# Kernel tuning notes

Measured on AMD Instinct MI355X. Metric: run time of the kernel, lower is better.

## Reference

```python
import jax, jax.numpy as jnp
import numpy as np

NEG_SLOPE = 0.2


def _segment_softmax(logits, seg, num_segments):
    m = jax.ops.segment_max(logits, seg, num_segments=num_segments)
    m = jnp.where(jnp.isfinite(m), m, 0.0)
    e = jnp.exp(logits - m[seg])
    s = jax.ops.segment_sum(e, seg, num_segments=num_segments)
    return e / (s[seg] + 1e-16)


def _gat_conv(x, src, dst, W, a_src, a_dst, b, num_nodes):
    # PyG GATConv, heads=1, concat=True, add_self_loops already applied to src/dst.
    h = x @ W                                  # [N, F_out]
    alpha_src = h @ a_src                      # [N]
    alpha_dst = h @ a_dst                      # [N]
    logits = jax.nn.leaky_relu(alpha_src[src] + alpha_dst[dst], NEG_SLOPE)  # [E]
    alpha = _segment_softmax(logits, dst, num_nodes)                        # [E]
    out = jax.ops.segment_sum(alpha[:, None] * h[src], dst, num_segments=num_nodes)
    return out + b


def setup_inputs() -> dict:
    key = jax.random.key(0)
    ks = jax.random.split(key, 16)
    N, E, F_in = 50000, 1600000, 256
    x = jax.random.normal(ks[0], (N, F_in), dtype=jnp.float32)
    edge_index = jax.random.randint(ks[1], (2, E), 0, N, dtype=jnp.int64)
    edge_attr = jax.random.normal(ks[2], (E, 1), dtype=jnp.float32)

    def glorot(k, shape):
        fan = sum(shape) if len(shape) > 1 else shape[0]
        return jax.random.normal(k, shape, dtype=jnp.float32) * jnp.sqrt(2.0 / fan)

    params = {
        "W1": glorot(ks[3], (F_in, 48)), "as1": glorot(ks[4], (48,)),
        "ad1": glorot(ks[5], (48,)),     "b1": jnp.zeros((48,), jnp.float32),
        "W2": glorot(ks[6], (48, 60)),   "as2": glorot(ks[7], (60,)),
        "ad2": glorot(ks[8], (60,)),     "b2": jnp.zeros((60,), jnp.float32),
        "W3": glorot(ks[9], (60, 1)),    "as3": glorot(ks[10], (1,)),
        "ad3": glorot(ks[11], (1,)),     "b3": jnp.zeros((1,), jnp.float32),
    }
    return {"x": x, "edge_index": edge_index, "edge_attr": edge_attr, **params}


def reference(x, edge_index, edge_attr, W1, as1, ad1, b1, W2, as2, ad2, b2, W3, as3, ad3, b3):
    # edge_attr is accepted but ignored: GATConv was built without edge_dim, so no lin_edge.
    N = x.shape[0]
    loops = jnp.arange(N, dtype=edge_index.dtype)
    src = jnp.concatenate([edge_index[0], loops])  # add_self_loops=True
    dst = jnp.concatenate([edge_index[1], loops])
    h = jax.nn.relu(_gat_conv(x, src, dst, W1, as1, ad1, b1, N))
    h = jax.nn.relu(_gat_conv(h, src, dst, W2, as2, ad2, b2, N))
    h = _gat_conv(h, src, dst, W3, as3, ad3, b3, N)
    return h.reshape(-1)  # flatten -> [N]
```

## Files before the change

kernel.cpp:

```cpp
#include <hip/hip_runtime.h>
#include <cstdint>
#include <cstddef>


__device__ __forceinline__ float leaky(float v) { return v > 0.f ? v : 0.2f * v; }

__device__ __forceinline__ unsigned short f2bf(float x) {
    unsigned int u = __float_as_uint(x);
    u = (u + 0x7FFFu + ((u >> 16) & 1u)) >> 16;
    return (unsigned short)u;
}
__device__ __forceinline__ float bf2f(unsigned short b) {
    return __uint_as_float(((unsigned int)b) << 16);
}

typedef _Float16 half8 __attribute__((ext_vector_type(8)));
typedef float f32x4 __attribute__((ext_vector_type(4)));

#define BSHIFT 7
#define BCAP   5120
#define CTILE  8192


__global__ __launch_bounds__(256) void coarse_bin_kernel(
    const int* __restrict__ ei, unsigned int* __restrict__ staged,
    int* __restrict__ gcursor, int E, int K) {
    __shared__ int hist[512];
    __shared__ int rank[512];
    __shared__ int base[512];
    for (int b = threadIdx.x; b < K; b += 256) { hist[b] = 0; rank[b] = 0; }
    __syncthreads();

    int e0 = blockIdx.x * CTILE;
    int e1 = min(E, e0 + CTILE);

    for (int e = e0 + threadIdx.x; e < e1; e += 256) {
        int d = ei[E + e];
        atomicAdd(&hist[d >> BSHIFT], 1);
    }
    __syncthreads();

    for (int b = threadIdx.x; b < K; b += 256) {
        int c = hist[b];
        base[b] = c ? atomicAdd(&gcursor[b], c) : 0;
    }
    __syncthreads();

    for (int e = e0 + threadIdx.x; e < e1; e += 256) {
        int s = ei[e];
        int d = ei[E + e];
        int b = d >> BSHIFT;
        int r = atomicAdd(&rank[b], 1);
        staged[(size_t)b * BCAP + base[b] + r] =
            ((unsigned int)(d & ((1 << BSHIFT) - 1)) << 16) | (unsigned int)s;
    }
}


__global__ __launch_bounds__(512) void bucket_scan_kernel(
    const int* __restrict__ gcursor, int* __restrict__ bbase, int K) {
    __shared__ int sh[512];
    int t = threadIdx.x;
    int v = (t < K) ? gcursor[t] : 0;
    sh[t] = v;
    __syncthreads();
    for (int off = 1; off < 512; off <<= 1) {
        int a = (t >= off) ? sh[t - off] : 0;
        __syncthreads();
        sh[t] += a;
        __syncthreads();
    }
    if (t < K) bbase[t] = sh[t] - v;
}


__global__ __launch_bounds__(256) void fine_sort_kernel(
    const unsigned int* __restrict__ staged, const int* __restrict__ gcursor,
    const int* __restrict__ bbase, int* __restrict__ rowptr, int* __restrict__ csr,
    int N, int E) {
    __shared__ int cnt[128];
    __shared__ int off[128];
    __shared__ int lcsr[BCAP];
    const int b = blockIdx.x;
    const int t = threadIdx.x;
    const int c = gcursor[b];
    const int gb = bbase[b];
    const unsigned int* rec = staged + (size_t)b * BCAP;

    if (t < 128) cnt[t] = 0;
    __syncthreads();

    for (int i = t; i < c; i += 256) atomicAdd(&cnt[rec[i] >> 16], 1);
    __syncthreads();

    if (t < 128) off[t] = cnt[t];
    __syncthreads();
    for (int s = 1; s < 128; s <<= 1) {
        int a = (t >= s && t < 128) ? off[t - s] : 0;
        __syncthreads();
        if (t < 128) off[t] += a;
        __syncthreads();
    }

    if (t < 128) {
        int excl = off[t] - cnt[t];
        int n = (b << BSHIFT) + t;
        if (n <= N) rowptr[n] = gb + excl;
        cnt[t] = excl;
    }
    if (b == 0 && t == 0) rowptr[N] = E;
    __syncthreads();

    for (int i = t; i < c; i += 256) {
        unsigned int r = rec[i];
        int p = atomicAdd(&cnt[r >> 16], 1);
        lcsr[p] = (int)(r & 0xFFFFu);
    }
    __syncthreads();

    for (int i = t; i < c; i += 256) csr[gb + i] = lcsr[i];
}


template <int FIN>
__global__ __launch_bounds__(256) void gemm1_mfma_kernel(
    const float* __restrict__ X, const float* __restrict__ W,
    const float* __restrict__ avs, const float* __restrict__ avd,
    unsigned short* __restrict__ hb, float* __restrict__ asrc, float* __restrict__ adst,
    int N) {
    constexpr int FOUT = 48;
    constexpr int KK = FIN / 32;
    static_assert(FIN % 32 == 0, "FIN multiple of 32");

    const int wid  = __builtin_amdgcn_readfirstlane(threadIdx.x >> 6);
    const int lane = threadIdx.x & 63;
    const int col  = lane & 15;
    const int grp  = lane >> 4;
    const int wbase = blockIdx.x * 64 + wid * 16;

    int arow = wbase + col;
    if (arow >= N) arow = N - 1;
    const float* xrow = X + (size_t)arow * FIN + grp * 8;

    half8 Bf[3][KK];
#pragma unroll
    for (int t = 0; t < 3; t++) {
#pragma unroll
        for (int kk = 0; kk < KK; kk++) {
            const float* wp = W + (size_t)(kk * 32 + grp * 8) * FOUT + t * 16 + col;
#pragma unroll
            for (int j = 0; j < 8; j++)
                Bf[t][kk][j] = (_Float16)wp[(size_t)j * FOUT];
        }
    }

    f32x4 acc0 = {0.f, 0.f, 0.f, 0.f};
    f32x4 acc1 = {0.f, 0.f, 0.f, 0.f};
    f32x4 acc2 = {0.f, 0.f, 0.f, 0.f};

#pragma unroll
    for (int kk = 0; kk < KK; kk++) {
        float4 xa = *(const float4*)(xrow + kk * 32);
        float4 xb = *(const float4*)(xrow + kk * 32 + 4);
        float xs[8] = {xa.x, xa.y, xa.z, xa.w, xb.x, xb.y, xb.z, xb.w};
        half8 ah, al;
#pragma unroll
        for (int j = 0; j < 8; j++) {
            _Float16 h = (_Float16)xs[j];
            ah[j] = h;
            al[j] = (_Float16)(xs[j] - (float)h);
        }
        acc0 = __builtin_amdgcn_mfma_f32_16x16x32_f16(ah, Bf[0][kk], acc0, 0, 0, 0);
        acc1 = __builtin_amdgcn_mfma_f32_16x16x32_f16(ah, Bf[1][kk], acc1, 0, 0, 0);
        acc2 = __builtin_amdgcn_mfma_f32_16x16x32_f16(ah, Bf[2][kk], acc2, 0, 0, 0);
        acc0 = __builtin_amdgcn_mfma_f32_16x16x32_f16(al, Bf[0][kk], acc0, 0, 0, 0);
        acc1 = __builtin_amdgcn_mfma_f32_16x16x32_f16(al, Bf[1][kk], acc1, 0, 0, 0);
        acc2 = __builtin_amdgcn_mfma_f32_16x16x32_f16(al, Bf[2][kk], acc2, 0, 0, 0);
    }

    float avs0 = avs[col], avs1 = avs[16 + col], avs2 = avs[32 + col];
    float avd0 = avd[col], avd1 = avd[16 + col], avd2 = avd[32 + col];

#pragma unroll
    for (int r = 0; r < 4; r++) {
        float ps = acc0[r] * avs0 + acc1[r] * avs1 + acc2[r] * avs2;
        float pd = acc0[r] * avd0 + acc1[r] * avd1 + acc2[r] * avd2;
#pragma unroll
        for (int off = 8; off; off >>= 1) {
            ps += __shfl_xor(ps, off, 64);
            pd += __shfl_xor(pd, off, 64);
        }
        int nd = wbase + grp * 4 + r;
        if (col == r && nd < N) { asrc[nd] = ps; adst[nd] = pd; }
    }

#pragma unroll
    for (int r = 0; r < 4; r++) {
        int nd = wbase + grp * 4 + r;
        if (nd < N) {
            unsigned short* hp = hb + (size_t)nd * 64 + col;
            hp[0]  = f2bf(acc0[r]);
            hp[16] = f2bf(acc1[r]);
            hp[32] = f2bf(acc2[r]);
        }
    }
}


template <int FIN, int FOUT, int FT>
__global__ __launch_bounds__(256) void gemm_sgpr_kernel(
    const float* __restrict__ X, const float* __restrict__ W,
    const float* __restrict__ avs, const float* __restrict__ avd,
    unsigned short* __restrict__ hb, float* __restrict__ asrc, float* __restrict__ adst,
    int N) {
    static_assert(4 * FT == FOUT, "FT must be FOUT/4");
    __shared__ float red[2][4][64];

    const int wid  = __builtin_amdgcn_readfirstlane(threadIdx.x >> 6);
    const int lane = threadIdx.x & 63;
    const int n    = blockIdx.x * 64 + lane;
    const int nc   = (n < N) ? n : N - 1;
    const int fbase = wid * FT;

    const float* xrow = X + (size_t)nc * FIN;

    float acc[FT];
#pragma unroll
    for (int c = 0; c < FT; c++) acc[c] = 0.f;

#pragma unroll
    for (int k = 0; k < FIN; k += 4) {
        float4 xv = *(const float4*)(xrow + k);
        const float* w0 = W + (size_t)k * FOUT + fbase;
#pragma unroll
        for (int c = 0; c < FT; c++) {
            acc[c] = fmaf(xv.x, w0[c],            acc[c]);
            acc[c] = fmaf(xv.y, w0[FOUT + c],     acc[c]);
            acc[c] = fmaf(xv.z, w0[2 * FOUT + c], acc[c]);
            acc[c] = fmaf(xv.w, w0[3 * FOUT + c], acc[c]);
        }
    }

    float ps = 0.f, pd = 0.f;
#pragma unroll
    for (int c = 0; c < FT; c++) {
        ps = fmaf(acc[c], avs[fbase + c], ps);
        pd = fmaf(acc[c], avd[fbase + c], pd);
    }
    red[0][wid][lane] = ps;
    red[1][wid][lane] = pd;

    if (n < N) {
        if constexpr ((FT & 1) == 0) {
            unsigned int* dst = (unsigned int*)(hb + (size_t)n * 64 + fbase);
#pragma unroll
            for (int c = 0; c < FT; c += 2) {
                unsigned int pk = (unsigned int)f2bf(acc[c]) |
                                  ((unsigned int)f2bf(acc[c + 1]) << 16);
                dst[c >> 1] = pk;
            }
        } else {
#pragma unroll
            for (int c = 0; c < FT; c++)
                hb[(size_t)n * 64 + fbase + c] = f2bf(acc[c]);
        }
    }

    __syncthreads();
    if (threadIdx.x < 64 && n < N) {
        float s = red[0][0][lane] + red[0][1][lane] + red[0][2][lane] + red[0][3][lane];
        float d = red[1][0][lane] + red[1][1][lane] + red[1][2][lane] + red[1][3][lane];
        asrc[n] = s;
        adst[n] = d;
    }
}


#define CHUNK 128

template <int FOUT, bool RELU>
__global__ __launch_bounds__(256) void agg_bf16_kernel(
    const int* __restrict__ rowptr, const int* __restrict__ csr,
    const float* __restrict__ asrc, const float* __restrict__ adst,
    const unsigned short* __restrict__ hb, const float* __restrict__ bias,
    float* __restrict__ OUT, int N) {
    __shared__ int2 wslds[4][CHUNK];
    const int wv = threadIdx.x >> 6;
    int n = blockIdx.x * 4 + wv;
    if (n >= N) return;
    const int lane = threadIdx.x & 63;
    const int rs = rowptr[n], re = rowptr[n + 1];
    const float ad_n = adst[n];
    const float wself = __expf(leaky(asrc[n] + ad_n));
    const int fc = (lane < FOUT) ? lane : FOUT - 1;

    float acc = wself * bf2f(hb[(size_t)n * 64 + fc]);
    float wpart = 0.f;

    for (int base = rs; base < re; base += CHUNK) {
        const int cnt = min(CHUNK, re - base);
        if (lane < cnt) {
            int s = csr[base + lane];
            float w = __expf(leaky(asrc[s] + ad_n));
            wpart += w;
            wslds[wv][lane] = make_int2(s, __float_as_int(w));
        }
        int i = 0;
        for (; i + 8 <= cnt; i += 8) {
            int2 p[8];
#pragma unroll
            for (int u = 0; u < 8; u++) p[u] = wslds[wv][i + u];
            float hv[8];
#pragma unroll
            for (int u = 0; u < 8; u++) hv[u] = bf2f(hb[(size_t)p[u].x * 64 + fc]);
#pragma unroll
            for (int u = 0; u < 8; u++) acc = fmaf(__int_as_float(p[u].y), hv[u], acc);
        }
        for (; i < cnt; i++) {
            int2 pp = wslds[wv][i];
            acc = fmaf(__int_as_float(pp.y), bf2f(hb[(size_t)pp.x * 64 + fc]), acc);
        }
    }

#pragma unroll
    for (int off = 32; off; off >>= 1) wpart += __shfl_xor(wpart, off, 64);
    float ssum = wpart + wself;

    if (lane < FOUT) {
        float o = acc / (ssum + 1e-16f) + bias[lane];
        if (RELU) o = fmaxf(o, 0.f);
        OUT[(size_t)n * FOUT + lane] = o;
    }
}


__global__ __launch_bounds__(256) void agg_bf16_h3_kernel(
    const int* __restrict__ rowptr, const int* __restrict__ csr,
    const float* __restrict__ asrc, const float* __restrict__ adst,
    const unsigned short* __restrict__ hb, const float* __restrict__ bias,
    const float* __restrict__ W3, float* __restrict__ h3, int N) {
    constexpr int FOUT = 60;
    __shared__ int2 wslds[4][CHUNK];
    const int wv = threadIdx.x >> 6;
    int n = blockIdx.x * 4 + wv;
    if (n >= N) return;
    const int lane = threadIdx.x & 63;
    const int rs = rowptr[n], re = rowptr[n + 1];
    const float ad_n = adst[n];
    const float wself = __expf(leaky(asrc[n] + ad_n));
    const int fc = (lane < FOUT) ? lane : FOUT - 1;

    float acc = wself * bf2f(hb[(size_t)n * 64 + fc]);
    float wpart = 0.f;

    for (int base = rs; base < re; base += CHUNK) {
        const int cnt = min(CHUNK, re - base);
        if (lane < cnt) {
            int s = csr[base + lane];
            float w = __expf(leaky(asrc[s] + ad_n));
            wpart += w;
            wslds[wv][lane] = make_int2(s, __float_as_int(w));
        }
        int i = 0;
        for (; i + 8 <= cnt; i += 8) {
            int2 p[8];
#pragma unroll
            for (int u = 0; u < 8; u++) p[u] = wslds[wv][i + u];
            float hv[8];
#pragma unroll
            for (int u = 0; u < 8; u++) hv[u] = bf2f(hb[(size_t)p[u].x * 64 + fc]);
#pragma unroll
            for (int u = 0; u < 8; u++) acc = fmaf(__int_as_float(p[u].y), hv[u], acc);
        }
        for (; i < cnt; i++) {
            int2 pp = wslds[wv][i];
            acc = fmaf(__int_as_float(pp.y), bf2f(hb[(size_t)pp.x * 64 + fc]), acc);
        }
    }

#pragma unroll
    for (int off = 32; off; off >>= 1) wpart += __shfl_xor(wpart, off, 64);
    float ssum = wpart + wself;

    float t = 0.f;
    if (lane < FOUT) {
        float o = fmaxf(acc / (ssum + 1e-16f) + bias[lane], 0.f);
        t = o * W3[lane];
    }
#pragma unroll
    for (int off = 32; off; off >>= 1) t += __shfl_xor(t, off, 64);
    if (lane == 0) h3[n] = t;
}


__global__ __launch_bounds__(256) void agg1_kernel(
    const int* __restrict__ rowptr, const int* __restrict__ csr,
    const float* __restrict__ h3,
    const float* __restrict__ as3p, const float* __restrict__ ad3p,
    const float* __restrict__ bias, float* __restrict__ OUT, int N) {
    int n = blockIdx.x * 4 + (threadIdx.x >> 6);
    if (n >= N) return;
    int lane = threadIdx.x & 63;
    int rs = rowptr[n], re = rowptr[n + 1];
    const float a_s = as3p[0];
    float hn = h3[n];
    float adn = ad3p[0] * hn;
    float wself = __expf(leaky(a_s * hn + adn));

    float ssum = 0.f, accv = 0.f;
    for (int e = rs + lane; e < re; e += 64) {
        float hs = h3[csr[e]];
        float w = __expf(leaky(a_s * hs + adn));
        ssum += w;
        accv = fmaf(w, hs, accv);
    }
#pragma unroll
    for (int off = 32; off; off >>= 1) {
        ssum += __shfl_xor(ssum, off, 64);
        accv += __shfl_xor(accv, off, 64);
    }
    ssum += wself;
    accv = fmaf(wself, hn, accv);
    if (lane == 0) OUT[n] = accv / (ssum + 1e-16f) + bias[0];
}


extern "C" void kernel_launch(void* const* d_in, const int* in_sizes, int n_in,
                              void* d_out, int out_size, void* d_ws, size_t ws_size,
                              hipStream_t stream) {
    const float* x      = (const float*)d_in[0];
    const int*   ei     = (const int*)d_in[1];
    const float* W1  = (const float*)d_in[3];
    const float* as1 = (const float*)d_in[4];
    const float* ad1 = (const float*)d_in[5];
    const float* b1  = (const float*)d_in[6];
    const float* W2  = (const float*)d_in[7];
    const float* as2 = (const float*)d_in[8];
    const float* ad2 = (const float*)d_in[9];
    const float* b2  = (const float*)d_in[10];
    const float* W3  = (const float*)d_in[11];
    const float* as3 = (const float*)d_in[12];
    const float* ad3 = (const float*)d_in[13];
    const float* b3  = (const float*)d_in[14];

    const int N = in_sizes[0] / 256;
    const int E = in_sizes[1] / 2;
    const int K = (N + (1 << BSHIFT) - 1) >> BSHIFT;

    char* p = (char*)d_ws;
    auto alloc = [&](size_t bytes) -> void* {
        void* r = (void*)p;
        p += ((bytes + 255) / 256) * 256;
        return r;
    };
    int*   gcursor = (int*)alloc(512 * 4);
    int*   bbase   = (int*)alloc(512 * 4);
    int*   rowptr  = (int*)alloc(((size_t)N + 1) * 4);
    int*   csr     = (int*)alloc((size_t)E * 4);
    unsigned short* hb = (unsigned short*)alloc((size_t)N * 64 * 2);
    float* actbuf  = (float*)alloc((size_t)N * 48 * 4);
    float* h3      = (float*)alloc((size_t)N * 4);
    float* asrc    = (float*)alloc((size_t)N * 4);
    float* adst    = (float*)alloc((size_t)N * 4);
    unsigned int* staged = (unsigned int*)actbuf;

    hipMemsetAsync(gcursor, 0, 512 * 4, stream);
    int cblocks = (E + CTILE - 1) / CTILE;
    coarse_bin_kernel<<<cblocks, 256, 0, stream>>>(ei, staged, gcursor, E, K);
    bucket_scan_kernel<<<1, 512, 0, stream>>>(gcursor, bbase, K);
    fine_sort_kernel<<<K, 256, 0, stream>>>(staged, gcursor, bbase, rowptr, csr, N, E);

    int gblocks = (N + 63) / 64;
    int ablocks = (N + 3) / 4;

    gemm1_mfma_kernel<256><<<gblocks, 256, 0, stream>>>(
        x, W1, as1, ad1, hb, asrc, adst, N);
    agg_bf16_kernel<48, true><<<ablocks, 256, 0, stream>>>(rowptr, csr, asrc, adst, hb, b1, actbuf, N);

    gemm_sgpr_kernel<48, 60, 15><<<gblocks, 256, 0, stream>>>(
        actbuf, W2, as2, ad2, hb, asrc, adst, N);
    agg_bf16_h3_kernel<<<ablocks, 256, 0, stream>>>(rowptr, csr, asrc, adst, hb, b2, W3, h3, N);

    agg1_kernel<<<ablocks, 256, 0, stream>>>(rowptr, csr, h3, as3, ad3, b3, (float*)d_out, N);
}
```

Measured before the change: 285.3 us.

## Split wave into four edge groups with 8-byte bf16 feature loads in aggregation

Both aggregation kernels now give each quarter of the wave a different neighbor edge. Each lane loads 4 bf16 features (8 bytes) at once, instead of every lane loading a single feature for the same edge. Partial sums from the four groups are combined with cross-lane shuffles, and then the self-loop term is added. The goal is fewer memory instructions per edge and more edges gathered in flight. In exchange there is extra shuffle reduction, the tail edges need masked handling, and offsets are computed as 32-bit byte addresses.

```diff
diff --git a/kernel.cpp b/kernel.cpp
--- a/kernel.cpp
+++ b/kernel.cpp
@@ -12,6 +12,12 @@
 }
 __device__ __forceinline__ float bf2f(unsigned short b) {
     return __uint_as_float(((unsigned int)b) << 16);
+}
+__device__ __forceinline__ float bfhi(unsigned int d) {
+    return __uint_as_float(d & 0xFFFF0000u);
+}
+__device__ __forceinline__ float bflo(unsigned int d) {
+    return __uint_as_float(d << 16);
 }
 
 typedef _Float16 half8 __attribute__((ext_vector_type(8)));
@@ -279,22 +285,27 @@
 #define CHUNK 128
 
 template <int FOUT, bool RELU>
-__global__ __launch_bounds__(256) void agg_bf16_kernel(
+__global__ __launch_bounds__(256) void agg_quad_kernel(
     const int* __restrict__ rowptr, const int* __restrict__ csr,
     const float* __restrict__ asrc, const float* __restrict__ adst,
     const unsigned short* __restrict__ hb, const float* __restrict__ bias,
     float* __restrict__ OUT, int N) {
+    constexpr int NSUB = FOUT / 4;
+    static_assert(FOUT % 4 == 0, "FOUT multiple of 4");
     __shared__ int2 wslds[4][CHUNK];
     const int wv = threadIdx.x >> 6;
     int n = blockIdx.x * 4 + wv;
     if (n >= N) return;
     const int lane = threadIdx.x & 63;
+    const int q    = lane >> 4;
+    const int sub  = lane & 15;
+    const unsigned int suboff = (unsigned int)sub * 8;
     const int rs = rowptr[n], re = rowptr[n + 1];
     const float ad_n = adst[n];
     const float wself = __expf(leaky(asrc[n] + ad_n));
-    const int fc = (lane < FOUT) ? lane : FOUT - 1;
-
-    float acc = wself * bf2f(hb[(size_t)n * 64 + fc]);
+    const char* hbb = (const char*)hb;
+
+    float a0 = 0.f, a1 = 0.f, a2 = 0.f, a3 = 0.f;
     float wpart = 0.f;
 
     for (int base = rs; base < re; base += CHUNK) {
@@ -303,54 +314,85 @@
             int s = csr[base + lane];
             float w = __expf(leaky(asrc[s] + ad_n));
             wpart += w;
-            wslds[wv][lane] = make_int2(s, __float_as_int(w));
+            wslds[wv][lane] = make_int2(s << 7, __float_as_int(w));
         }
         int i = 0;
-        for (; i + 8 <= cnt; i += 8) {
-            int2 p[8];
-#pragma unroll
-            for (int u = 0; u < 8; u++) p[u] = wslds[wv][i + u];
-            float hv[8];
-#pragma unroll
-            for (int u = 0; u < 8; u++) hv[u] = bf2f(hb[(size_t)p[u].x * 64 + fc]);
-#pragma unroll
-            for (int u = 0; u < 8; u++) acc = fmaf(__int_as_float(p[u].y), hv[u], acc);
-        }
-        for (; i < cnt; i++) {
-            int2 pp = wslds[wv][i];
-            acc = fmaf(__int_as_float(pp.y), bf2f(hb[(size_t)pp.x * 64 + fc]), acc);
+        for (; i + 4 <= cnt; i += 4) {
+            int2 p = wslds[wv][i + q];
+            uint2 dv = *(const uint2*)(hbb + ((unsigned int)p.x + suboff));
+            float w = __int_as_float(p.y);
+            a0 = fmaf(w, bflo(dv.x), a0);
+            a1 = fmaf(w, bfhi(dv.x), a1);
+            a2 = fmaf(w, bflo(dv.y), a2);
+            a3 = fmaf(w, bfhi(dv.y), a3);
+        }
+        const int rem = cnt - i;
+        if (rem) {
+            int2 p = wslds[wv][i + ((q < rem) ? q : 0)];
+            uint2 dv = *(const uint2*)(hbb + ((unsigned int)p.x + suboff));
+            float w = (q < rem) ? __int_as_float(p.y) : 0.f;
+            a0 = fmaf(w, bflo(dv.x), a0);
+            a1 = fmaf(w, bfhi(dv.x), a1);
+            a2 = fmaf(w, bflo(dv.y), a2);
+            a3 = fmaf(w, bfhi(dv.y), a3);
         }
     }
 
 #pragma unroll
     for (int off = 32; off; off >>= 1) wpart += __shfl_xor(wpart, off, 64);
-    float ssum = wpart + wself;
-
-    if (lane < FOUT) {
-        float o = acc / (ssum + 1e-16f) + bias[lane];
-        if (RELU) o = fmaxf(o, 0.f);
-        OUT[(size_t)n * FOUT + lane] = o;
-    }
-}
-
-
-__global__ __launch_bounds__(256) void agg_bf16_h3_kernel(
+    const float ssum = wpart + wself;
+
+    a0 += __shfl_xor(a0, 16, 64); a0 += __shfl_xor(a0, 32, 64);
+    a1 += __shfl_xor(a1, 16, 64); a1 += __shfl_xor(a1, 32, 64);
+    a2 += __shfl_xor(a2, 16, 64); a2 += __shfl_xor(a2, 32, 64);
+    a3 += __shfl_xor(a3, 16, 64); a3 += __shfl_xor(a3, 32, 64);
+
+    {
+        uint2 sv = *(const uint2*)(hbb + (((unsigned int)n << 7) + suboff));
+        a0 = fmaf(wself, bflo(sv.x), a0);
+        a1 = fmaf(wself, bfhi(sv.x), a1);
+        a2 = fmaf(wself, bflo(sv.y), a2);
+        a3 = fmaf(wself, bfhi(sv.y), a3);
+    }
+
+    if (lane < NSUB) {
+        const float inv = 1.f / (ssum + 1e-16f);
+        float4 bv = *(const float4*)(bias + sub * 4);
+        float4 o;
+        o.x = a0 * inv + bv.x;
+        o.y = a1 * inv + bv.y;
+        o.z = a2 * inv + bv.z;
+        o.w = a3 * inv + bv.w;
+        if (RELU) {
+            o.x = fmaxf(o.x, 0.f); o.y = fmaxf(o.y, 0.f);
+            o.z = fmaxf(o.z, 0.f); o.w = fmaxf(o.w, 0.f);
+        }
+        *(float4*)(OUT + (size_t)n * FOUT + sub * 4) = o;
+    }
+}
+
+
+__global__ __launch_bounds__(256) void agg_quad_h3_kernel(
     const int* __restrict__ rowptr, const int* __restrict__ csr,
     const float* __restrict__ asrc, const float* __restrict__ adst,
     const unsigned short* __restrict__ hb, const float* __restrict__ bias,
     const float* __restrict__ W3, float* __restrict__ h3, int N) {
     constexpr int FOUT = 60;
+    constexpr int NSUB = FOUT / 4;
     __shared__ int2 wslds[4][CHUNK];
     const int wv = threadIdx.x >> 6;
     int n = blockIdx.x * 4 + wv;
     if (n >= N) return;
     const int lane = threadIdx.x & 63;
+    const int q    = lane >> 4;
+    const int sub  = lane & 15;
+    const unsigned int suboff = (unsigned int)sub * 8;
     const int rs = rowptr[n], re = rowptr[n + 1];
     const float ad_n = adst[n];
     const float wself = __expf(leaky(asrc[n] + ad_n));
-    const int fc = (lane < FOUT) ? lane : FOUT - 1;
-
-    float acc = wself * bf2f(hb[(size_t)n * 64 + fc]);
+    const char* hbb = (const char*)hb;
+
+    float a0 = 0.f, a1 = 0.f, a2 = 0.f, a3 = 0.f;
     float wpart = 0.f;
 
     for (int base = rs; base < re; base += CHUNK) {
@@ -359,36 +401,62 @@
             int s = csr[base + lane];
             float w = __expf(leaky(asrc[s] + ad_n));
             wpart += w;
-            wslds[wv][lane] = make_int2(s, __float_as_int(w));
+            wslds[wv][lane] = make_int2(s << 7, __float_as_int(w));
         }
         int i = 0;
-        for (; i + 8 <= cnt; i += 8) {
-            int2 p[8];
-#pragma unroll
-            for (int u = 0; u < 8; u++) p[u] = wslds[wv][i + u];
-            float hv[8];
-#pragma unroll
-            for (int u = 0; u < 8; u++) hv[u] = bf2f(hb[(size_t)p[u].x * 64 + fc]);
-#pragma unroll
-            for (int u = 0; u < 8; u++) acc = fmaf(__int_as_float(p[u].y), hv[u], acc);
-        }
-        for (; i < cnt; i++) {
-            int2 pp = wslds[wv][i];
-            acc = fmaf(__int_as_float(pp.y), bf2f(hb[(size_t)pp.x * 64 + fc]), acc);
+        for (; i + 4 <= cnt; i += 4) {
+            int2 p = wslds[wv][i + q];
+            uint2 dv = *(const uint2*)(hbb + ((unsigned int)p.x + suboff));
+            float w = __int_as_float(p.y);
+            a0 = fmaf(w, bflo(dv.x), a0);
+            a1 = fmaf(w, bfhi(dv.x), a1);
+            a2 = fmaf(w, bflo(dv.y), a2);
+            a3 = fmaf(w, bfhi(dv.y), a3);
+        }
+        const int rem = cnt - i;
+        if (rem) {
+            int2 p = wslds[wv][i + ((q < rem) ? q : 0)];
+            uint2 dv = *(const uint2*)(hbb + ((unsigned int)p.x + suboff));
+            float w = (q < rem) ? __int_as_float(p.y) : 0.f;
+            a0 = fmaf(w, bflo(dv.x), a0);
+            a1 = fmaf(w, bfhi(dv.x), a1);
+            a2 = fmaf(w, bflo(dv.y), a2);
+            a3 = fmaf(w, bfhi(dv.y), a3);
         }
     }
 
 #pragma unroll
     for (int off = 32; off; off >>= 1) wpart += __shfl_xor(wpart, off, 64);
-    float ssum = wpart + wself;
+    const float ssum = wpart + wself;
+
+    a0 += __shfl_xor(a0, 16, 64); a0 += __shfl_xor(a0, 32, 64);
+    a1 += __shfl_xor(a1, 16, 64); a1 += __shfl_xor(a1, 32, 64);
+    a2 += __shfl_xor(a2, 16, 64); a2 += __shfl_xor(a2, 32, 64);
+    a3 += __shfl_xor(a3, 16, 64); a3 += __shfl_xor(a3, 32, 64);
+
+    {
+        uint2 sv = *(const uint2*)(hbb + (((unsigned int)n << 7) + suboff));
+        a0 = fmaf(wself, bflo(sv.x), a0);
+        a1 = fmaf(wself, bfhi(sv.x), a1);
+        a2 = fmaf(wself, bflo(sv.y), a2);
+        a3 = fmaf(wself, bfhi(sv.y), a3);
+    }
 
     float t = 0.f;
-    if (lane < FOUT) {
-        float o = fmaxf(acc / (ssum + 1e-16f) + bias[lane], 0.f);
-        t = o * W3[lane];
-    }
-#pragma unroll
-    for (int off = 32; off; off >>= 1) t += __shfl_xor(t, off, 64);
+    {
+        const int subc = (sub < NSUB) ? sub : 0;
+        const float inv = 1.f / (ssum + 1e-16f);
+        float4 bv = *(const float4*)(bias + subc * 4);
+        float4 wv3 = *(const float4*)(W3 + subc * 4);
+        float o0 = fmaxf(a0 * inv + bv.x, 0.f);
+        float o1 = fmaxf(a1 * inv + bv.y, 0.f);
+        float o2 = fmaxf(a2 * inv + bv.z, 0.f);
+        float o3 = fmaxf(a3 * inv + bv.w, 0.f);
+        if (sub < NSUB)
+            t = o0 * wv3.x + o1 * wv3.y + o2 * wv3.z + o3 * wv3.w;
+    }
+#pragma unroll
+    for (int off = 8; off; off >>= 1) t += __shfl_xor(t, off, 64);
     if (lane == 0) h3[n] = t;
 }
 
@@ -475,11 +543,11 @@
 
     gemm1_mfma_kernel<256><<<gblocks, 256, 0, stream>>>(
         x, W1, as1, ad1, hb, asrc, adst, N);
-    agg_bf16_kernel<48, true><<<ablocks, 256, 0, stream>>>(rowptr, csr, asrc, adst, hb, b1, actbuf, N);
+    agg_quad_kernel<48, true><<<ablocks, 256, 0, stream>>>(rowptr, csr, asrc, adst, hb, b1, actbuf, N);
 
     gemm_sgpr_kernel<48, 60, 15><<<gblocks, 256, 0, stream>>>(
         actbuf, W2, as2, ad2, hb, asrc, adst, N);
-    agg_bf16_h3_kernel<<<ablocks, 256, 0, stream>>>(rowptr, csr, asrc, adst, hb, b2, W3, h3, N);
+    agg_quad_h3_kernel<<<ablocks, 256, 0, stream>>>(rowptr, csr, asrc, adst, hb, b2, W3, h3, N);
 
     agg1_kernel<<<ablocks, 256, 0, stream>>>(rowptr, csr, h3, as3, ad3, b3, (float*)d_out, N);
 }
```

Result: no change. 283.6 us (-0.6%).
